# Optimization experiments

Hardware: AMD Instinct MI355X
Metric: run time of the kernel (lower is better)

## Reference

```python
import jax, jax.numpy as jnp
import numpy as np
import math

# Static problem sizes (match input_specs)
B, TQ, SQ, TK, SK = 1, 8, 256, 32, 1024
DM, NH = 1024, 8
HD = DM // NH            # 128; mrope_section sums to HD//2
MROPE = [16, 24, 24]
ROPE_BASE = 10000.0


def _build_indices():
    """Reproduce create_idx_cube + slow/fast index selection (all static)."""
    T_max = max(TQ, TK)
    H_max = int(math.sqrt(max(SQ, SK)))
    cube = np.stack(np.meshgrid(np.arange(T_max), np.arange(H_max), np.arange(H_max), indexing='ij'), axis=-1)  # (T,H,W,3)
    # slow (query) indices
    t_idx = np.linspace(0, T_max - 1, TQ).astype(int)
    slow = cube[t_idx]
    if SQ < SK:
        h_q = int(math.sqrt(SQ))
        hi = np.linspace(0, H_max, 2 * h_q + 1).astype(int)[1:-1][::2]
        slow = slow[:, hi][:, :, hi]
    # fast (key) indices
    h_k = int(math.sqrt(SK))
    hf = np.linspace(0, H_max, 2 * h_k + 1).astype(int)[1:-1][::2]
    fast = cube[:, hf][:, :, hf]
    return slow.reshape(-1, 3).T, fast.reshape(-1, 3).T, max(T_max, H_max)


_slow_np, _fast_np, _SEQ = _build_indices()
SLOW_POS = jnp.asarray(_slow_np)   # (3, TQ*SQ) int
FAST_POS = jnp.asarray(_fast_np)   # (3, TK*SK) int

# Standard rotary tables: cos/sin of shape (seq_len, HD)
_inv = 1.0 / (ROPE_BASE ** (np.arange(0, HD, 2, dtype=np.float32) / HD))
_freqs = np.outer(np.arange(_SEQ, dtype=np.float32), _inv)
_emb = np.concatenate([_freqs, _freqs], axis=-1)
COS = jnp.asarray(np.cos(_emb), dtype=jnp.float32)
SIN = jnp.asarray(np.sin(_emb), dtype=jnp.float32)

# per-channel axis (t/h/w) selector, equivalent to the split/concat with i%3
AXIS_MAP = jnp.asarray(np.concatenate([np.full(m, i % 3) for i, m in enumerate(MROPE * 2)]))  # (HD,)


def rotate_half(x):
    return jnp.concatenate([-x[..., HD // 2:], x[..., :HD // 2]], axis=-1)


def apply_mrope(x, pos):
    # x: (B, NH, N, HD); pos: (3, N)
    cos_g = jnp.take_along_axis(COS[pos], AXIS_MAP[None, None, :], axis=0)[0]  # (N, HD)
    sin_g = jnp.take_along_axis(SIN[pos], AXIS_MAP[None, None, :], axis=0)[0]
    return x * cos_g[None, None] + rotate_half(x) * sin_g[None, None]


def setup_inputs() -> dict:
    key = jax.random.key(0)
    ks = jax.random.split(key, 9)
    s = 0.02
    return {
        'q': jax.random.normal(ks[0], (B, TQ, SQ, DM), jnp.float32),
        'k': jax.random.normal(ks[1], (B, TK, SK, DM), jnp.float32),
        'v': jax.random.normal(ks[2], (B, TK, SK, DM), jnp.float32),
        'Wq': jax.random.normal(ks[3], (DM, DM), jnp.float32) * s,
        'bq': jnp.zeros((DM,), jnp.float32),
        'Wk': jax.random.normal(ks[4], (DM, DM), jnp.float32) * s,
        'bk': jnp.zeros((DM,), jnp.float32),
        'Wv': jax.random.normal(ks[5], (DM, DM), jnp.float32) * s,
        'bv': jnp.zeros((DM,), jnp.float32),
    }


def reference(q, k, v, Wq, bq, Wk, bk, Wv, bv):
    # QKV projections -> (B, NH, N, HD)
    qh = (q.reshape(B, TQ * SQ, DM) @ Wq + bq).reshape(B, TQ * SQ, NH, HD).transpose(0, 2, 1, 3)
    kh = (k.reshape(B, TK * SK, DM) @ Wk + bk).reshape(B, TK * SK, NH, HD).transpose(0, 2, 1, 3)
    vh = (v.reshape(B, TK * SK, DM) @ Wv + bv).reshape(B, TK * SK, NH, HD).transpose(0, 2, 1, 3)
    # multimodal 3D RoPE on q (slow frames) and k (fast frames)
    qh = apply_mrope(qh, SLOW_POS)
    kh = apply_mrope(kh, FAST_POS)
    # group time: each query frame attends to its r = TK//TQ aligned kv frames
    r = TK // TQ
    qg = qh.reshape(NH, TQ, SQ, HD).transpose(1, 0, 2, 3)          # (TQ, NH, SQ, HD)
    kg = kh.reshape(NH, TQ, r * SK, HD).transpose(1, 0, 2, 3)      # (TQ, NH, r*SK, HD)
    vg = vh.reshape(NH, TQ, r * SK, HD).transpose(1, 0, 2, 3)
    scores = jnp.einsum('thqd,thkd->thqk', qg, kg) / math.sqrt(HD)
    attn = jax.nn.softmax(scores, axis=-1)
    out = jnp.einsum('thqk,thkd->thqd', attn, vg)                  # (TQ, NH, SQ, HD)
    return out.transpose(0, 2, 1, 3).reshape(B, TQ, SQ, DM)
```

## Files before the change

kernel.cpp:

```cpp
#include <hip/hip_runtime.h>

typedef __bf16 bf16;
typedef __bf16 bf16x8 __attribute__((ext_vector_type(8)));
typedef float  f32x4  __attribute__((ext_vector_type(4)));

#define MFMA16(a, b, c) __builtin_amdgcn_mfma_f32_16x16x32_bf16((a), (b), (c), 0, 0, 0)

#define GLOAD_LDS16(gptr, lptr)                                              \
    __builtin_amdgcn_global_load_lds(                                        \
        (const __attribute__((address_space(1))) unsigned int*)(gptr),       \
        (__attribute__((address_space(3))) unsigned int*)(lptr), 16, 0, 0)

constexpr int kDM = 1024;
constexpr int kNTOK = 32768;

static __device__ inline f32x4 zero4() { f32x4 z = {0.f, 0.f, 0.f, 0.f}; return z; }

__global__ __launch_bounds__(256) void convert_bf16(
    const float* __restrict__ in, bf16* __restrict__ out)
{
    const size_t i = ((size_t)blockIdx.x * 256 + threadIdx.x) * 8;
    float4 a = *(const float4*)&in[i];
    float4 b = *(const float4*)&in[i + 4];
    bf16 t[8];
    t[0] = (bf16)a.x; t[1] = (bf16)a.y; t[2] = (bf16)a.z; t[3] = (bf16)a.w;
    t[4] = (bf16)b.x; t[5] = (bf16)b.y; t[6] = (bf16)b.z; t[7] = (bf16)b.w;
    *(uint4*)&out[i] = *(const uint4*)t;
}

__global__ __launch_bounds__(256) void transpose_w(
    const float* __restrict__ W, bf16* __restrict__ Wt)
{
    __shared__ bf16 T[64][68];
    const int tid = threadIdx.x;
    const int n0 = blockIdx.x * 64, k0 = blockIdx.y * 64;
    #pragma unroll
    for (int i = 0; i < 4; i++) {
        const int kk = (tid >> 4) + i * 16, nn4 = (tid & 15) * 4;
        float4 v = *(const float4*)&W[(size_t)(k0 + kk) * kDM + n0 + nn4];
        T[nn4 + 0][kk] = (bf16)v.x; T[nn4 + 1][kk] = (bf16)v.y;
        T[nn4 + 2][kk] = (bf16)v.z; T[nn4 + 3][kk] = (bf16)v.w;
    }
    __syncthreads();
    #pragma unroll
    for (int i = 0; i < 4; i++) {
        const int nn = (tid >> 4) + i * 16, kc = (tid & 15) * 4;
        *(ushort4*)&Wt[(size_t)(n0 + nn) * kDM + k0 + kc] = *(const ushort4*)&T[nn][kc];
    }
}

template <bool TRANSPOSED>
__global__ __launch_bounds__(256) void gemm_bt(
    const bf16* __restrict__ Xb, const bf16* __restrict__ Wt,
    const float* __restrict__ bias, bf16* __restrict__ out, int mtiles_per_xcd)
{
    __shared__ char smem[TRANSPOSED ? 34816 : 32768];
    bf16* Ab = (bf16*)smem;
    bf16* Bb = (bf16*)(smem + 16384);

    const int b    = blockIdx.x;
    const int xcd  = b & 7;
    const int s    = b >> 3;
    const int m0   = (xcd * mtiles_per_xcd + (s >> 3)) * 128;
    const int n0   = (s & 7) * 128;
    const int tid  = threadIdx.x;
    const int wave = tid >> 6;
    const int lane = tid & 63;
    const int quad = lane >> 4, l16 = lane & 15;
    const int mb   = (wave & 1) * 64, nb = (wave >> 1) * 64;
    const int r8   = lane >> 3, j8 = lane & 7;
    const int sw8  = (j8 ^ r8) * 8;

    f32x4 acc[4][4];
    #pragma unroll
    for (int i = 0; i < 4; i++)
        #pragma unroll
        for (int j = 0; j < 4; j++) acc[i][j] = zero4();

    for (int k0 = 0; k0 < kDM; k0 += 64) {
        __syncthreads();
        #pragma unroll
        for (int i = 0; i < 4; i++) {
            const int c = wave * 4 + i;
            GLOAD_LDS16(&Xb[(size_t)(m0 + c * 8 + r8) * kDM + k0 + sw8], &Ab[c * 512]);
        }
        #pragma unroll
        for (int i = 0; i < 4; i++) {
            const int c = wave * 4 + i;
            GLOAD_LDS16(&Wt[(size_t)(n0 + c * 8 + r8) * kDM + k0 + sw8], &Bb[c * 512]);
        }
        __syncthreads();
        #pragma unroll
        for (int ks = 0; ks < 2; ks++) {
            bf16x8 a[4], bfr[4];
            #pragma unroll
            for (int i = 0; i < 4; i++) {
                const int m = mb + i * 16 + l16;
                a[i] = *(const bf16x8*)&Ab[m * 64 + (((ks * 4 + quad) ^ (l16 & 7)) * 8)];
            }
            #pragma unroll
            for (int j = 0; j < 4; j++) {
                const int n = nb + j * 16 + l16;
                bfr[j] = *(const bf16x8*)&Bb[n * 64 + (((ks * 4 + quad) ^ (l16 & 7)) * 8)];
            }
            #pragma unroll
            for (int i = 0; i < 4; i++)
                #pragma unroll
                for (int j = 0; j < 4; j++)
                    acc[i][j] = MFMA16(a[i], bfr[j], acc[i][j]);
        }
    }

    if (!TRANSPOSED) {
        #pragma unroll
        for (int j = 0; j < 4; j++) {
            const int n = n0 + nb + j * 16 + l16;
            const float bv = bias[n];
            #pragma unroll
            for (int i = 0; i < 4; i++)
                #pragma unroll
                for (int r = 0; r < 4; r++) {
                    const int m = m0 + mb + i * 16 + quad * 4 + r;
                    out[(size_t)m * kDM + n] = (bf16)(acc[i][j][r] + bv);
                }
        }
    } else {
        __syncthreads();
        bf16* T = (bf16*)smem;
        #pragma unroll
        for (int j = 0; j < 4; j++) {
            const int n = nb + j * 16 + l16;
            const float bv = bias[n0 + n];
            #pragma unroll
            for (int i = 0; i < 4; i++) {
                const int m = mb + i * 16 + quad * 4;
                bf16 tmp[4];
                #pragma unroll
                for (int r = 0; r < 4; r++) tmp[r] = (bf16)(acc[i][j][r] + bv);
                *(ushort4*)&T[n * 136 + m] = *(const ushort4*)tmp;
            }
        }
        __syncthreads();
        const int row = tid >> 1, seg = (tid & 1) * 64;
        #pragma unroll
        for (int kk = 0; kk < 8; kk++)
            *(uint4*)&out[(size_t)(n0 + row) * kNTOK + m0 + seg + kk * 8] =
                *(const uint4*)&T[row * 136 + seg + kk * 8];
    }
}

__global__ __launch_bounds__(256) void rope_kernel(bf16* __restrict__ buf, int fast)
{
    const int gid = blockIdx.x * 256 + threadIdx.x;
    const int d = gid & 63;
    const int h = (gid >> 6) & 7;
    const int n = gid >> 9;
    int pt, ph, pw;
    if (fast) { pt = n >> 10; ph = (n >> 5) & 31; pw = n & 31; }
    else      { int tq = n >> 8; pt = (31 * tq) / 7; ph = 2 * ((n >> 4) & 15) + 1; pw = 2 * (n & 15) + 1; }
    const int p = (d < 16) ? pt : ((d < 40) ? ph : pw);
    const float angle = (float)p * exp2f((float)d * -0.20762050593045951f);
    const float c = cosf(angle), s = sinf(angle);
    const size_t i1 = (size_t)n * kDM + h * 128 + d;
    const float x1 = (float)buf[i1], x2 = (float)buf[i1 + 64];
    buf[i1]      = (bf16)(x1 * c - x2 * s);
    buf[i1 + 64] = (bf16)(x2 * c + x1 * s);
}

__global__ __launch_bounds__(256) void attn_kernel(
    const bf16* __restrict__ qh, const bf16* __restrict__ kh,
    const bf16* __restrict__ vt, float* __restrict__ Opart, float* __restrict__ ml)
{
    __shared__ bf16 Ks[64 * 128];
    __shared__ bf16 Vs[144 * 64];
    __shared__ bf16 Ps[4][16][72];

    const int tid  = threadIdx.x;
    const int z    = blockIdx.x, h = blockIdx.y, qb = blockIdx.z;
    const int t    = z >> 3, sp = z & 7;
    const int wave = tid >> 6;
    const int lane = tid & 63;
    const int quad = lane >> 4, l16 = lane & 15;

    for (int i = tid; i < 16 * 64; i += 256) Vs[(128 + (i >> 6)) * 64 + (i & 63)] = (bf16)1.0f;

    const int qrow = qb * 64 + wave * 16 + l16;
    const size_t qbase = ((size_t)(t * 256 + qrow)) * kDM + h * 128;
    bf16x8 aq[4];
    #pragma unroll
    for (int kb = 0; kb < 4; kb++)
        aq[kb] = *(const bf16x8*)&qh[qbase + kb * 32 + quad * 8];

    f32x4 o[9];
    #pragma unroll
    for (int j = 0; j < 9; j++) o[j] = zero4();
    float m_run[4];
    #pragma unroll
    for (int r = 0; r < 4; r++) m_run[r] = -1e30f;
    const float scale = 0.08838834764831845f;

    const int r16 = lane >> 4, j16 = lane & 15;
    const int r8  = lane >> 3, j8  = lane & 7;

    for (int kt = 0; kt < 8; kt++) {
        const int kbase = t * 4096 + sp * 512 + kt * 64;
        __syncthreads();
        #pragma unroll
        for (int i = 0; i < 4; i++) {
            const int c = wave * 4 + i;
            const int krow = c * 4 + r16;
            GLOAD_LDS16(&kh[(size_t)(kbase + krow) * kDM + h * 128 + ((j16 ^ (krow & 15)) * 8)],
                        &Ks[c * 512]);
        }
        #pragma unroll
        for (int i = 0; i < 4; i++) {
            const int c = wave * 4 + i;
            GLOAD_LDS16(&vt[(size_t)(h * 128 + c * 8 + r8) * kNTOK + kbase + ((j8 ^ r8) * 8)],
                        &Vs[c * 512]);
        }
        __syncthreads();

        f32x4 s[4];
        #pragma unroll
        for (int c = 0; c < 4; c++) s[c] = zero4();
        #pragma unroll
        for (int kb = 0; kb < 4; kb++) {
            #pragma unroll
            for (int c = 0; c < 4; c++) {
                bf16x8 b = *(const bf16x8*)&Ks[(c * 16 + l16) * 128 + (((kb * 4 + quad) ^ l16) * 8)];
                s[c] = MFMA16(aq[kb], b, s[c]);
            }
        }

        float alpha[4];
        #pragma unroll
        for (int r = 0; r < 4; r++) {
            float sv[4];
            #pragma unroll
            for (int c = 0; c < 4; c++) sv[c] = s[c][r] * scale;
            float mx = fmaxf(fmaxf(sv[0], sv[1]), fmaxf(sv[2], sv[3]));
            #pragma unroll
            for (int off = 1; off < 16; off <<= 1) mx = fmaxf(mx, __shfl_xor(mx, off));
            const float mn = fmaxf(m_run[r], mx);
            alpha[r] = __expf(m_run[r] - mn);
            m_run[r] = mn;
            #pragma unroll
            for (int c = 0; c < 4; c++)
                Ps[wave][quad * 4 + r][c * 16 + l16] = (bf16)__expf(sv[c] - mn);
        }
        #pragma unroll
        for (int j = 0; j < 9; j++)
            #pragma unroll
            for (int r = 0; r < 4; r++) o[j][r] *= alpha[r];
        #pragma unroll
        for (int ks = 0; ks < 2; ks++) {
            bf16x8 pa = *(const bf16x8*)&Ps[wave][l16][ks * 32 + quad * 8];
            #pragma unroll
            for (int j = 0; j < 9; j++) {
                bf16x8 bv = *(const bf16x8*)&Vs[(j * 16 + l16) * 64 + (((ks * 4 + quad) ^ (l16 & 7)) * 8)];
                o[j] = MFMA16(pa, bv, o[j]);
            }
        }
    }

    #pragma unroll
    for (int r = 0; r < 4; r++) {
        const int srow = qb * 64 + wave * 16 + quad * 4 + r;
        const size_t pr = ((size_t)(z * 8 + h)) * 256 + srow;
        #pragma unroll
        for (int j = 0; j < 8; j++)
            Opart[pr * 128 + j * 16 + l16] = o[j][r];
        if (l16 == 0) { ml[pr * 2] = m_run[r]; ml[pr * 2 + 1] = o[8][r]; }
    }
}

__global__ __launch_bounds__(256) void combine_kernel(
    const float* __restrict__ Opart, const float* __restrict__ ml,
    float* __restrict__ out)
{
    const int tid = threadIdx.x;
    const int rid = blockIdx.x * 2 + (tid >> 7);
    const int d   = tid & 127;
    const int t = rid >> 11, h = (rid >> 8) & 7, srow = rid & 255;

    float mv[8], lv[8];
    #pragma unroll
    for (int sp = 0; sp < 8; sp++) {
        const size_t pr = ((size_t)((t * 8 + sp) * 8 + h)) * 256 + srow;
        float2 p = *(const float2*)&ml[pr * 2];
        mv[sp] = p.x; lv[sp] = p.y;
    }
    float ms = mv[0];
    #pragma unroll
    for (int sp = 1; sp < 8; sp++) ms = fmaxf(ms, mv[sp]);
    float lsum = 0.f, acc = 0.f;
    #pragma unroll
    for (int sp = 0; sp < 8; sp++) {
        const size_t pr = ((size_t)((t * 8 + sp) * 8 + h)) * 256 + srow;
        const float w = __expf(mv[sp] - ms);
        lsum += lv[sp] * w;
        acc  += Opart[pr * 128 + d] * w;
    }
    out[((size_t)(t * 256 + srow)) * kDM + h * 128 + d] = acc / lsum;
}

extern "C" void kernel_launch(void* const* d_in, const int* in_sizes, int n_in,
                              void* d_out, int out_size, void* d_ws, size_t ws_size,
                              hipStream_t stream)
{
    const float* q  = (const float*)d_in[0];
    const float* k  = (const float*)d_in[1];
    const float* v  = (const float*)d_in[2];
    const float* Wq = (const float*)d_in[3];
    const float* bq = (const float*)d_in[4];
    const float* Wk = (const float*)d_in[5];
    const float* bk = (const float*)d_in[6];
    const float* Wv = (const float*)d_in[7];
    const float* bv = (const float*)d_in[8];
    float* out = (float*)d_out;

    bf16* qh  = (bf16*)d_ws;
    bf16* kh  = qh + (size_t)2048 * 1024;
    bf16* vt  = kh + (size_t)32768 * 1024;
    bf16* Wqt = vt + (size_t)32768 * 1024;
    bf16* Wkt = Wqt + (size_t)1024 * 1024;
    bf16* Wvt = Wkt + (size_t)1024 * 1024;
    bf16* qb_  = Wvt + (size_t)1024 * 1024;
    bf16* kb_  = qb_ + (size_t)2048 * 1024;
    bf16* vb_  = kb_ + (size_t)32768 * 1024;
    float* Opart = (float*)kb_;
    float* ml    = Opart + (size_t)64 * 8 * 256 * 128;

    convert_bf16<<<1024,  256, 0, stream>>>(q, qb_);
    convert_bf16<<<16384, 256, 0, stream>>>(k, kb_);
    convert_bf16<<<16384, 256, 0, stream>>>(v, vb_);
    transpose_w<<<dim3(16, 16), 256, 0, stream>>>(Wq, Wqt);
    transpose_w<<<dim3(16, 16), 256, 0, stream>>>(Wk, Wkt);
    transpose_w<<<dim3(16, 16), 256, 0, stream>>>(Wv, Wvt);
    gemm_bt<false><<<128,  256, 0, stream>>>(qb_, Wqt, bq, qh, 2);
    gemm_bt<false><<<2048, 256, 0, stream>>>(kb_, Wkt, bk, kh, 32);
    gemm_bt<true><<<2048,  256, 0, stream>>>(vb_, Wvt, bv, vt, 32);
    rope_kernel<<<4096,  256, 0, stream>>>(qh, 0);
    rope_kernel<<<65536, 256, 0, stream>>>(kh, 1);
    attn_kernel<<<dim3(64, 8, 4), 256, 0, stream>>>(qh, kh, vt, Opart, ml);
    combine_kernel<<<8192, 256, 0, stream>>>(Opart, ml, out);
}
```

Baseline: 701.6 us.

## Fuse input conversion and RoPE into projection GEMMs, halve attention KV splits

The separate fp32-to-bf16 conversion kernels are removed. The GEMM now loads fp32 activations straight into LDS and converts them to bf16 while building MFMA fragments. The standalone RoPE kernels are folded into the Q/K GEMM epilogue, which stages the tile in LDS and applies the rotation with __sincosf before a coalesced store. The three weight transposes become one launch, and the attention split over the KV dimension drops from 8 to 4 partitions, with a register 'ones' operand for the row sum and a swizzled P buffer. These changes cut intermediate traffic and launches, at the cost of doubled fp32 A-tile LDS, lower attention grid parallelism, and a less precise sincos.

```diff
diff --git a/kernel.cpp b/kernel.cpp
--- a/kernel.cpp
+++ b/kernel.cpp
@@ -16,22 +16,14 @@
 
 static __device__ inline f32x4 zero4() { f32x4 z = {0.f, 0.f, 0.f, 0.f}; return z; }
 
-__global__ __launch_bounds__(256) void convert_bf16(
-    const float* __restrict__ in, bf16* __restrict__ out)
-{
-    const size_t i = ((size_t)blockIdx.x * 256 + threadIdx.x) * 8;
-    float4 a = *(const float4*)&in[i];
-    float4 b = *(const float4*)&in[i + 4];
-    bf16 t[8];
-    t[0] = (bf16)a.x; t[1] = (bf16)a.y; t[2] = (bf16)a.z; t[3] = (bf16)a.w;
-    t[4] = (bf16)b.x; t[5] = (bf16)b.y; t[6] = (bf16)b.z; t[7] = (bf16)b.w;
-    *(uint4*)&out[i] = *(const uint4*)t;
-}
-
-__global__ __launch_bounds__(256) void transpose_w(
-    const float* __restrict__ W, bf16* __restrict__ Wt)
+__global__ __launch_bounds__(256) void transpose_all(
+    const float* __restrict__ Wq, const float* __restrict__ Wk,
+    const float* __restrict__ Wv, bf16* __restrict__ Wqt,
+    bf16* __restrict__ Wkt, bf16* __restrict__ Wvt)
 {
     __shared__ bf16 T[64][68];
+    const float* W = (blockIdx.z == 0) ? Wq : (blockIdx.z == 1) ? Wk : Wv;
+    bf16* Wt       = (blockIdx.z == 0) ? Wqt : (blockIdx.z == 1) ? Wkt : Wvt;
     const int tid = threadIdx.x;
     const int n0 = blockIdx.x * 64, k0 = blockIdx.y * 64;
     #pragma unroll
@@ -49,14 +41,15 @@
     }
 }
 
-template <bool TRANSPOSED>
-__global__ __launch_bounds__(256) void gemm_bt(
-    const bf16* __restrict__ Xb, const bf16* __restrict__ Wt,
+template <int MODE>
+__global__ __launch_bounds__(256) void gemm_fused(
+    const float* __restrict__ X, const bf16* __restrict__ Wt,
     const float* __restrict__ bias, bf16* __restrict__ out, int mtiles_per_xcd)
 {
-    __shared__ char smem[TRANSPOSED ? 34816 : 32768];
-    bf16* Ab = (bf16*)smem;
-    bf16* Bb = (bf16*)(smem + 16384);
+    __shared__ char smem[49152];
+    float* Af = (float*)smem;
+    bf16*  Bb = (bf16*)(smem + 32768);
+    bf16*  Y  = (bf16*)smem;
 
     const int b    = blockIdx.x;
     const int xcd  = b & 7;
@@ -68,8 +61,6 @@
     const int lane = tid & 63;
     const int quad = lane >> 4, l16 = lane & 15;
     const int mb   = (wave & 1) * 64, nb = (wave >> 1) * 64;
-    const int r8   = lane >> 3, j8 = lane & 7;
-    const int sw8  = (j8 ^ r8) * 8;
 
     f32x4 acc[4][4];
     #pragma unroll
@@ -79,15 +70,20 @@
 
     for (int k0 = 0; k0 < kDM; k0 += 64) {
         __syncthreads();
+        #pragma unroll
+        for (int i = 0; i < 8; i++) {
+            const int c = wave * 8 + i;
+            const int row = c * 4 + (lane >> 4);
+            const int sl  = lane & 15;
+            const int src = ((((sl >> 1) ^ (row & 7)) << 1) | (sl & 1)) * 4;
+            GLOAD_LDS16(&X[(size_t)(m0 + row) * kDM + k0 + src], &Af[c * 256]);
+        }
         #pragma unroll
         for (int i = 0; i < 4; i++) {
             const int c = wave * 4 + i;
-            GLOAD_LDS16(&Xb[(size_t)(m0 + c * 8 + r8) * kDM + k0 + sw8], &Ab[c * 512]);
-        }
-        #pragma unroll
-        for (int i = 0; i < 4; i++) {
-            const int c = wave * 4 + i;
-            GLOAD_LDS16(&Wt[(size_t)(n0 + c * 8 + r8) * kDM + k0 + sw8], &Bb[c * 512]);
+            const int row = c * 8 + (lane >> 3);
+            GLOAD_LDS16(&Wt[(size_t)(n0 + row) * kDM + k0 + (((lane & 7) ^ (row & 7)) * 8)],
+                        &Bb[c * 512]);
         }
         __syncthreads();
         #pragma unroll
@@ -96,7 +92,12 @@
             #pragma unroll
             for (int i = 0; i < 4; i++) {
                 const int m = mb + i * 16 + l16;
-                a[i] = *(const bf16x8*)&Ab[m * 64 + (((ks * 4 + quad) ^ (l16 & 7)) * 8)];
+                const int G = (ks * 4 + quad) ^ (l16 & 7);
+                const float* p = &Af[m * 64 + G * 8];
+                f32x4 u0 = *(const f32x4*)p;
+                f32x4 u1 = *(const f32x4*)(p + 4);
+                #pragma unroll
+                for (int e = 0; e < 4; e++) { a[i][e] = (bf16)u0[e]; a[i][4 + e] = (bf16)u1[e]; }
             }
             #pragma unroll
             for (int j = 0; j < 4; j++) {
@@ -111,22 +112,9 @@
         }
     }
 
-    if (!TRANSPOSED) {
-        #pragma unroll
-        for (int j = 0; j < 4; j++) {
-            const int n = n0 + nb + j * 16 + l16;
-            const float bv = bias[n];
-            #pragma unroll
-            for (int i = 0; i < 4; i++)
-                #pragma unroll
-                for (int r = 0; r < 4; r++) {
-                    const int m = m0 + mb + i * 16 + quad * 4 + r;
-                    out[(size_t)m * kDM + n] = (bf16)(acc[i][j][r] + bv);
-                }
-        }
-    } else {
-        __syncthreads();
-        bf16* T = (bf16*)smem;
+    __syncthreads();
+
+    if (MODE == 3) {
         #pragma unroll
         for (int j = 0; j < 4; j++) {
             const int n = nb + j * 16 + l16;
@@ -137,7 +125,7 @@
                 bf16 tmp[4];
                 #pragma unroll
                 for (int r = 0; r < 4; r++) tmp[r] = (bf16)(acc[i][j][r] + bv);
-                *(ushort4*)&T[n * 136 + m] = *(const ushort4*)tmp;
+                *(ushort4*)&Y[n * 136 + m] = *(const ushort4*)tmp;
             }
         }
         __syncthreads();
@@ -145,26 +133,56 @@
         #pragma unroll
         for (int kk = 0; kk < 8; kk++)
             *(uint4*)&out[(size_t)(n0 + row) * kNTOK + m0 + seg + kk * 8] =
-                *(const uint4*)&T[row * 136 + seg + kk * 8];
-    }
-}
-
-__global__ __launch_bounds__(256) void rope_kernel(bf16* __restrict__ buf, int fast)
-{
-    const int gid = blockIdx.x * 256 + threadIdx.x;
-    const int d = gid & 63;
-    const int h = (gid >> 6) & 7;
-    const int n = gid >> 9;
-    int pt, ph, pw;
-    if (fast) { pt = n >> 10; ph = (n >> 5) & 31; pw = n & 31; }
-    else      { int tq = n >> 8; pt = (31 * tq) / 7; ph = 2 * ((n >> 4) & 15) + 1; pw = 2 * (n & 15) + 1; }
-    const int p = (d < 16) ? pt : ((d < 40) ? ph : pw);
-    const float angle = (float)p * exp2f((float)d * -0.20762050593045951f);
-    const float c = cosf(angle), s = sinf(angle);
-    const size_t i1 = (size_t)n * kDM + h * 128 + d;
-    const float x1 = (float)buf[i1], x2 = (float)buf[i1 + 64];
-    buf[i1]      = (bf16)(x1 * c - x2 * s);
-    buf[i1 + 64] = (bf16)(x2 * c + x1 * s);
+                *(const uint4*)&Y[row * 136 + seg + kk * 8];
+    } else {
+        if (wave >= 2) {
+            #pragma unroll
+            for (int j = 0; j < 4; j++) {
+                const int dcol = 64 + j * 16 + l16;
+                const float bv = bias[n0 + dcol];
+                #pragma unroll
+                for (int i = 0; i < 4; i++)
+                    #pragma unroll
+                    for (int r = 0; r < 4; r++)
+                        Y[(mb + i * 16 + quad * 4 + r) * 136 + dcol] =
+                            (bf16)(acc[i][j][r] + bv);
+            }
+        }
+        __syncthreads();
+        if (wave < 2) {
+            #pragma unroll
+            for (int j = 0; j < 4; j++) {
+                const int d = j * 16 + l16;
+                const float bv = bias[n0 + d];
+                const float invf = exp2f((float)d * -0.20762050593045951f);
+                #pragma unroll
+                for (int i = 0; i < 4; i++) {
+                    #pragma unroll
+                    for (int r = 0; r < 4; r++) {
+                        const int mloc = mb + i * 16 + quad * 4 + r;
+                        const int tok = m0 + mloc;
+                        int pt, ph, pw;
+                        if (MODE == 2) { pt = tok >> 10; ph = (tok >> 5) & 31; pw = tok & 31; }
+                        else { int tq = tok >> 8; pt = (31 * tq) / 7;
+                               ph = 2 * ((tok >> 4) & 15) + 1; pw = 2 * (tok & 15) + 1; }
+                        const int p = (d < 16) ? pt : ((d < 40) ? ph : pw);
+                        float sn, cs;
+                        __sincosf((float)p * invf, &sn, &cs);
+                        const float x1 = acc[i][j][r] + bv;
+                        const float x2 = (float)Y[mloc * 136 + 64 + d];
+                        Y[mloc * 136 + d]      = (bf16)(x1 * cs - x2 * sn);
+                        Y[mloc * 136 + 64 + d] = (bf16)(x2 * cs + x1 * sn);
+                    }
+                }
+            }
+        }
+        __syncthreads();
+        const int row = tid >> 1, seg = (tid & 1) * 64;
+        #pragma unroll
+        for (int kk = 0; kk < 8; kk++)
+            *(uint4*)&out[(size_t)(m0 + row) * kDM + n0 + seg + kk * 8] =
+                *(const uint4*)&Y[row * 136 + seg + kk * 8];
+    }
 }
 
 __global__ __launch_bounds__(256) void attn_kernel(
@@ -172,18 +190,16 @@
     const bf16* __restrict__ vt, float* __restrict__ Opart, float* __restrict__ ml)
 {
     __shared__ bf16 Ks[64 * 128];
-    __shared__ bf16 Vs[144 * 64];
-    __shared__ bf16 Ps[4][16][72];
+    __shared__ bf16 Vs[128 * 64];
+    __shared__ bf16 Ps[4][16][64];
 
     const int tid  = threadIdx.x;
     const int z    = blockIdx.x, h = blockIdx.y, qb = blockIdx.z;
-    const int t    = z >> 3, sp = z & 7;
+    const int t    = z >> 2, sp = z & 3;
     const int wave = tid >> 6;
     const int lane = tid & 63;
     const int quad = lane >> 4, l16 = lane & 15;
 
-    for (int i = tid; i < 16 * 64; i += 256) Vs[(128 + (i >> 6)) * 64 + (i & 63)] = (bf16)1.0f;
-
     const int qrow = qb * 64 + wave * 16 + l16;
     const size_t qbase = ((size_t)(t * 256 + qrow)) * kDM + h * 128;
     bf16x8 aq[4];
@@ -191,6 +207,10 @@
     for (int kb = 0; kb < 4; kb++)
         aq[kb] = *(const bf16x8*)&qh[qbase + kb * 32 + quad * 8];
 
+    bf16x8 ones;
+    #pragma unroll
+    for (int e = 0; e < 8; e++) ones[e] = (bf16)1.0f;
+
     f32x4 o[9];
     #pragma unroll
     for (int j = 0; j < 9; j++) o[j] = zero4();
@@ -202,8 +222,8 @@
     const int r16 = lane >> 4, j16 = lane & 15;
     const int r8  = lane >> 3, j8  = lane & 7;
 
-    for (int kt = 0; kt < 8; kt++) {
-        const int kbase = t * 4096 + sp * 512 + kt * 64;
+    for (int kt = 0; kt < 16; kt++) {
+        const int kbase = t * 4096 + sp * 1024 + kt * 64;
         __syncthreads();
         #pragma unroll
         for (int i = 0; i < 4; i++) {
@@ -244,9 +264,12 @@
             const float mn = fmaxf(m_run[r], mx);
             alpha[r] = __expf(m_run[r] - mn);
             m_run[r] = mn;
-            #pragma unroll
-            for (int c = 0; c < 4; c++)
-                Ps[wave][quad * 4 + r][c * 16 + l16] = (bf16)__expf(sv[c] - mn);
+            const int q7 = quad * 4 + r;
+            #pragma unroll
+            for (int c = 0; c < 4; c++) {
+                const int col = (c * 16 + l16) ^ ((q7 & 7) * 8);
+                Ps[wave][q7][col] = (bf16)__expf(sv[c] - mn);
+            }
         }
         #pragma unroll
         for (int j = 0; j < 9; j++)
@@ -254,12 +277,13 @@
             for (int r = 0; r < 4; r++) o[j][r] *= alpha[r];
         #pragma unroll
         for (int ks = 0; ks < 2; ks++) {
-            bf16x8 pa = *(const bf16x8*)&Ps[wave][l16][ks * 32 + quad * 8];
-            #pragma unroll
-            for (int j = 0; j < 9; j++) {
+            bf16x8 pa = *(const bf16x8*)&Ps[wave][l16][((ks * 4 + quad) ^ (l16 & 7)) * 8];
+            #pragma unroll
+            for (int j = 0; j < 8; j++) {
                 bf16x8 bv = *(const bf16x8*)&Vs[(j * 16 + l16) * 64 + (((ks * 4 + quad) ^ (l16 & 7)) * 8)];
                 o[j] = MFMA16(pa, bv, o[j]);
             }
+            o[8] = MFMA16(pa, ones, o[8]);
         }
     }
 
@@ -283,20 +307,18 @@
     const int d   = tid & 127;
     const int t = rid >> 11, h = (rid >> 8) & 7, srow = rid & 255;
 
-    float mv[8], lv[8];
-    #pragma unroll
-    for (int sp = 0; sp < 8; sp++) {
-        const size_t pr = ((size_t)((t * 8 + sp) * 8 + h)) * 256 + srow;
+    float mv[4], lv[4];
+    #pragma unroll
+    for (int sp = 0; sp < 4; sp++) {
+        const size_t pr = ((size_t)((t * 4 + sp) * 8 + h)) * 256 + srow;
         float2 p = *(const float2*)&ml[pr * 2];
         mv[sp] = p.x; lv[sp] = p.y;
     }
-    float ms = mv[0];
-    #pragma unroll
-    for (int sp = 1; sp < 8; sp++) ms = fmaxf(ms, mv[sp]);
+    const float ms = fmaxf(fmaxf(mv[0], mv[1]), fmaxf(mv[2], mv[3]));
     float lsum = 0.f, acc = 0.f;
     #pragma unroll
-    for (int sp = 0; sp < 8; sp++) {
-        const size_t pr = ((size_t)((t * 8 + sp) * 8 + h)) * 256 + srow;
+    for (int sp = 0; sp < 4; sp++) {
+        const size_t pr = ((size_t)((t * 4 + sp) * 8 + h)) * 256 + srow;
         const float w = __expf(mv[sp] - ms);
         lsum += lv[sp] * w;
         acc  += Opart[pr * 128 + d] * w;
@@ -325,23 +347,13 @@
     bf16* Wqt = vt + (size_t)32768 * 1024;
     bf16* Wkt = Wqt + (size_t)1024 * 1024;
     bf16* Wvt = Wkt + (size_t)1024 * 1024;
-    bf16* qb_  = Wvt + (size_t)1024 * 1024;
-    bf16* kb_  = qb_ + (size_t)2048 * 1024;
-    bf16* vb_  = kb_ + (size_t)32768 * 1024;
-    float* Opart = (float*)kb_;
-    float* ml    = Opart + (size_t)64 * 8 * 256 * 128;
-
-    convert_bf16<<<1024,  256, 0, stream>>>(q, qb_);
-    convert_bf16<<<16384, 256, 0, stream>>>(k, kb_);
-    convert_bf16<<<16384, 256, 0, stream>>>(v, vb_);
-    transpose_w<<<dim3(16, 16), 256, 0, stream>>>(Wq, Wqt);
-    transpose_w<<<dim3(16, 16), 256, 0, stream>>>(Wk, Wkt);
-    transpose_w<<<dim3(16, 16), 256, 0, stream>>>(Wv, Wvt);
-    gemm_bt<false><<<128,  256, 0, stream>>>(qb_, Wqt, bq, qh, 2);
-    gemm_bt<false><<<2048, 256, 0, stream>>>(kb_, Wkt, bk, kh, 32);
-    gemm_bt<true><<<2048,  256, 0, stream>>>(vb_, Wvt, bv, vt, 32);
-    rope_kernel<<<4096,  256, 0, stream>>>(qh, 0);
-    rope_kernel<<<65536, 256, 0, stream>>>(kh, 1);
-    attn_kernel<<<dim3(64, 8, 4), 256, 0, stream>>>(qh, kh, vt, Opart, ml);
+    float* Opart = (float*)(Wvt + (size_t)1024 * 1024);
+    float* ml    = Opart + (size_t)32 * 8 * 256 * 128;
+
+    transpose_all<<<dim3(16, 16, 3), 256, 0, stream>>>(Wq, Wk, Wv, Wqt, Wkt, Wvt);
+    gemm_fused<1><<<128,  256, 0, stream>>>(q, Wqt, bq, qh, 2);
+    gemm_fused<2><<<2048, 256, 0, stream>>>(k, Wkt, bk, kh, 32);
+    gemm_fused<3><<<2048, 256, 0, stream>>>(v, Wvt, bv, vt, 32);
+    attn_kernel<<<dim3(32, 8, 4), 256, 0, stream>>>(qh, kh, vt, Opart, ml);
     combine_kernel<<<8192, 256, 0, stream>>>(Opart, ml, out);
 }
```

Result: faster. 641.0 us (-8.6%).
